# Kernel tuning notes

Hardware: AMD Instinct MI355X
Metric: run time of the kernel (lower is better)

Reference implementation:

```python
import jax, jax.numpy as jnp
import numpy as np

N, E, F_IN, HID, L, G, FFN = 100000, 1600000, 64, 128, 4, 512, 300
BN_EPS = 1e-5


def setup_inputs() -> dict:
    key = jax.random.key(0)
    ks = jax.random.split(key, 16)
    s = 0.05
    inp = {}
    inp["x"] = jax.random.normal(ks[0], (N, F_IN), dtype=jnp.float32)
    inp["edge_index"] = jax.random.randint(ks[1], (2, E), 0, N)
    inp["batch"] = jnp.sort(jax.random.randint(ks[2], (N,), 0, G))
    inp["enc_W"] = jax.random.normal(ks[3], (F_IN, HID), dtype=jnp.float32) * s
    inp["enc_b"] = jnp.zeros((HID,), jnp.float32)
    inp["Ws"] = jax.random.normal(ks[4], (L, HID, HID), dtype=jnp.float32) * s
    inp["bs"] = jnp.zeros((L, HID), jnp.float32)
    inp["bn_gamma"] = jnp.ones((L, HID), jnp.float32)
    inp["bn_beta"] = jnp.zeros((L, HID), jnp.float32)
    inp["bn_mean"] = jax.random.normal(ks[5], (L, HID), dtype=jnp.float32) * 0.01
    inp["bn_var"] = jnp.ones((L, HID), jnp.float32)
    inp["mlp_W0"] = jax.random.normal(ks[6], (HID, FFN), dtype=jnp.float32) * s
    inp["mlp_b0"] = jnp.zeros((FFN,), jnp.float32)
    inp["mlp_W1"] = jax.random.normal(ks[7], (FFN, FFN), dtype=jnp.float32) * s
    inp["mlp_b1"] = jnp.zeros((FFN,), jnp.float32)
    inp["mlp_W2"] = jax.random.normal(ks[8], (FFN, 1), dtype=jnp.float32) * s
    inp["mlp_b2"] = jnp.zeros((1,), jnp.float32)
    return inp


def reference(x, edge_index, batch, enc_W, enc_b, Ws, bs, bn_gamma, bn_beta,
              bn_mean, bn_var, mlp_W0, mlp_b0, mlp_W1, mlp_b1, mlp_W2, mlp_b2):
    # --- GCN normalization with self-loops (constant wrt params) ---
    loop = jnp.arange(N)
    row = jnp.concatenate([edge_index[0], loop])  # source
    col = jnp.concatenate([edge_index[1], loop])  # target (aggregation)
    deg = jax.ops.segment_sum(jnp.ones((E + N,), jnp.float32), col, num_segments=N)
    dinv = jnp.where(deg > 0, jax.lax.rsqrt(deg), 0.0)
    norm = dinv[row] * dinv[col]  # [E+N]

    # node encoder
    h = x @ enc_W + enc_b  # [N, HID]

    for i in range(L):
        h_prev = h
        # GCNConv: D^-1/2 (A+I) D^-1/2 (h W) + b
        hw = h @ Ws[i]
        msg = norm[:, None] * hw[row]                      # [E+N, HID]
        h = jax.ops.segment_sum(msg, col, num_segments=N) + bs[i]
        # BatchNorm1d (eval mode, running stats)
        h = (h - bn_mean[i]) * jax.lax.rsqrt(bn_var[i] + BN_EPS) * bn_gamma[i] + bn_beta[i]
        h = jax.nn.relu(h)
        if i > 0:
            h = h + h_prev

    # global mean pool over graphs
    sums = jax.ops.segment_sum(h, batch, num_segments=G)   # [G, HID]
    cnts = jax.ops.segment_sum(jnp.ones((N,), jnp.float32), batch, num_segments=G)
    gfeat = sums / jnp.maximum(cnts, 1.0)[:, None]

    # output MLP
    o = jax.nn.relu(gfeat @ mlp_W0 + mlp_b0)
    o = jax.nn.relu(o @ mlp_W1 + mlp_b1)
    return o @ mlp_W2 + mlp_b2  # [G, 1]
```

## Files before the change

kernel.cpp:

```cpp
#include <hip/hip_runtime.h>
#include <hip/hip_fp16.h>

#define NN 100000
#define NE 1600000
#define FIN 64
#define HID 128
#define NL 4
#define NG 512
#define FFN 300
#define BN_EPS 1e-5f
#define LDH 136
#define NB 512
#define NPB 196
#define CURPAD 16
#define CAP 4096

static inline size_t alignup(size_t x) { return (x + 255) & ~(size_t)255; }

struct half8 { __half2 h[4]; };

typedef _Float16 f16;
typedef __attribute__((ext_vector_type(4))) _Float16 f16x4;
typedef __attribute__((ext_vector_type(8))) _Float16 f16x8;
typedef __attribute__((ext_vector_type(4))) float f32x4;

__global__ void k_initcur(int* __restrict__ bcur) {
    int t = threadIdx.x;
    if (t < NB) bcur[t * CURPAD] = t * CAP;
}

__global__ __launch_bounds__(1024) void k_bscatter2(const int* __restrict__ row,
                                                    const int* __restrict__ col,
                                                    int* __restrict__ bcur,
                                                    int* __restrict__ ebuf) {
    __shared__ int hcnt[NB];
    __shared__ int hbase[NB];
    int t = threadIdx.x;
    int e0 = blockIdx.x * 4096;
    if (t < NB) hcnt[t] = 0;
    __syncthreads();
    #pragma unroll
    for (int k = 0; k < 4; ++k) {
        int e = e0 + k * 1024 + t;
        if (e < NE) atomicAdd(&hcnt[col[e] / NPB], 1);
    }
    __syncthreads();
    if (t < NB) {
        int c = hcnt[t];
        hbase[t] = (c > 0) ? atomicAdd(&bcur[t * CURPAD], c) : 0;
    }
    __syncthreads();
    if (t < NB) hcnt[t] = 0;
    __syncthreads();
    #pragma unroll
    for (int k = 0; k < 4; ++k) {
        int e = e0 + k * 1024 + t;
        if (e < NE) {
            int c = col[e];
            int b = c / NPB;
            int loc = atomicAdd(&hcnt[b], 1);
            ebuf[hbase[b] + loc] = row[e] | ((c - b * NPB) << 17);
        }
    }
}

__global__ __launch_bounds__(256) void k_binfill(const int* __restrict__ ebuf,
                                                 const int* __restrict__ bcur,
                                                 int* __restrict__ offs,
                                                 int* __restrict__ ends,
                                                 float* __restrict__ dinv,
                                                 int* __restrict__ csr_src) {
    __shared__ int cnt[NPB];
    __shared__ int scn[256];
    __shared__ int cur[NPB];
    int b = blockIdx.x, t = threadIdx.x;
    int lo = b * NPB;
    int hi = lo + NPB; if (hi > NN) hi = NN;
    int n = hi - lo;
    if (n <= 0) return;
    int s0 = b * CAP;
    int s1 = bcur[b * CURPAD];
    for (int i = t; i < NPB; i += 256) cnt[i] = 0;
    __syncthreads();
    for (int j = s0 + t; j < s1; j += 256)
        atomicAdd(&cnt[((unsigned)ebuf[j]) >> 17], 1);
    __syncthreads();
    int v = (t < n) ? cnt[t] : 0;
    scn[t] = v;
    __syncthreads();
    for (int off = 1; off < 256; off <<= 1) {
        int u = (t >= off) ? scn[t - off] : 0;
        __syncthreads();
        scn[t] += u;
        __syncthreads();
    }
    if (t < n) {
        int g = s0 + scn[t] - v;
        offs[lo + t] = g;
        ends[lo + t] = g + v;
        dinv[lo + t] = rsqrtf((float)(v + 1));
        cur[t] = g;
    }
    __syncthreads();
    for (int j = s0 + t; j < s1; j += 256) {
        int e = ebuf[j];
        int pos = atomicAdd(&cur[((unsigned)e) >> 17], 1);
        csr_src[pos] = e & 0x1FFFF;
    }
}

__global__ void k_convW(const float* __restrict__ Ws, const float* __restrict__ encW,
                        const float* __restrict__ bs, const float* __restrict__ gam,
                        const float* __restrict__ bet, const float* __restrict__ mean,
                        const float* __restrict__ var,
                        f16* __restrict__ wt, f16* __restrict__ wte,
                        float* __restrict__ pscale, float* __restrict__ pshift) {
    int tid = blockIdx.x * 256 + threadIdx.x;
    for (int i = tid; i < NL * HID * HID; i += 64 * 256) {
        int l = i >> 14, rem = i & 16383;
        int c = rem >> 7, k = rem & 127;
        wt[i] = (f16)Ws[(l << 14) + k * HID + c];
    }
    for (int i = tid; i < HID * FIN; i += 64 * 256) {
        int c = i >> 6, k = i & 63;
        wte[i] = (f16)encW[k * HID + c];
    }
    for (int i = tid; i < NL * HID; i += 64 * 256) {
        float rs = rsqrtf(var[i] + BN_EPS) * gam[i];
        pscale[i] = rs;
        pshift[i] = (bs[i] - mean[i]) * rs + bet[i];
    }
}

__global__ __launch_bounds__(256) void k_enc_mfma(const float* __restrict__ x,
                                                  const f16* __restrict__ wte,
                                                  const float* __restrict__ b,
                                                  __half* __restrict__ h) {
    __shared__ f16 sx[64 * 72];
    __shared__ f16 sw[128 * 72];
    int t = threadIdx.x;
    int row0 = blockIdx.x * 64;
    for (int idx = t; idx < 64 * 16; idx += 256) {
        int r = idx >> 4, c4 = (idx & 15) * 4;
        float4 v = {0.0f, 0.0f, 0.0f, 0.0f};
        if (row0 + r < NN) v = *(const float4*)(x + (size_t)(row0 + r) * FIN + c4);
        f16x4 o = {(f16)v.x, (f16)v.y, (f16)v.z, (f16)v.w};
        *(f16x4*)&sx[r * 72 + c4] = o;
    }
    for (int idx = t; idx < 128 * 8; idx += 256) {
        int c = idx >> 3, ch = (idx & 7) * 8;
        *(f16x8*)&sw[c * 72 + ch] = *(const f16x8*)(wte + c * FIN + ch);
    }
    __syncthreads();
    int w = t >> 6, lane = t & 63;
    int lrow = lane & 15, lk = (lane >> 4) * 8;
    f32x4 acc[8];
    #pragma unroll
    for (int ct = 0; ct < 8; ++ct) acc[ct] = (f32x4){0.0f, 0.0f, 0.0f, 0.0f};
    const f16* pa = &sx[(w * 16 + lrow) * 72 + lk];
    #pragma unroll
    for (int ks = 0; ks < 2; ++ks) {
        f16x8 a = *(const f16x8*)(pa + ks * 32);
        #pragma unroll
        for (int ct = 0; ct < 8; ++ct) {
            f16x8 bb = *(const f16x8*)&sw[(ct * 16 + lrow) * 72 + ks * 32 + lk];
            acc[ct] = __builtin_amdgcn_mfma_f32_16x16x32_f16(a, bb, acc[ct], 0, 0, 0);
        }
    }
    float bv[8];
    #pragma unroll
    for (int ct = 0; ct < 8; ++ct) bv[ct] = b[ct * 16 + lrow];
    int rbase = row0 + w * 16 + (lane >> 4) * 4;
    #pragma unroll
    for (int i = 0; i < 4; ++i) {
        int grow = rbase + i;
        if (grow < NN) {
            #pragma unroll
            for (int ct = 0; ct < 8; ++ct)
                h[(size_t)grow * HID + ct * 16 + lrow] = __float2half(acc[ct][i] + bv[ct]);
        }
    }
}

__global__ __launch_bounds__(256) void k_gemm_mfma(const __half* __restrict__ h,
                                                   const f16* __restrict__ wt,
                                                   const float* __restrict__ dinv,
                                                   __half* __restrict__ hw) {
    __shared__ f16 sh[64 * LDH];
    __shared__ f16 sw[128 * LDH];
    int t = threadIdx.x;
    int row0 = blockIdx.x * 64;
    for (int idx = t; idx < 64 * 16; idx += 256) {
        int r = idx >> 4, ch = (idx & 15) * 8;
        f16x8 v = {0, 0, 0, 0, 0, 0, 0, 0};
        if (row0 + r < NN) v = *(const f16x8*)(h + (size_t)(row0 + r) * HID + ch);
        *(f16x8*)&sh[r * LDH + ch] = v;
    }
    for (int idx = t; idx < 128 * 16; idx += 256) {
        int c = idx >> 4, ch = (idx & 15) * 8;
        *(f16x8*)&sw[c * LDH + ch] = *(const f16x8*)(wt + c * HID + ch);
    }
    __syncthreads();
    int w = t >> 6, lane = t & 63;
    int lrow = lane & 15, lk = (lane >> 4) * 8;
    f32x4 acc[8];
    #pragma unroll
    for (int ct = 0; ct < 8; ++ct) acc[ct] = (f32x4){0.0f, 0.0f, 0.0f, 0.0f};
    const f16* pa = &sh[(w * 16 + lrow) * LDH + lk];
    #pragma unroll
    for (int ks = 0; ks < 4; ++ks) {
        f16x8 a = *(const f16x8*)(pa + ks * 32);
        #pragma unroll
        for (int ct = 0; ct < 8; ++ct) {
            f16x8 b = *(const f16x8*)&sw[(ct * 16 + lrow) * LDH + ks * 32 + lk];
            acc[ct] = __builtin_amdgcn_mfma_f32_16x16x32_f16(a, b, acc[ct], 0, 0, 0);
        }
    }
    int rbase = row0 + w * 16 + (lane >> 4) * 4;
    #pragma unroll
    for (int i = 0; i < 4; ++i) {
        int grow = rbase + i;
        if (grow < NN) {
            float dv = dinv[grow];
            #pragma unroll
            for (int ct = 0; ct < 8; ++ct)
                hw[(size_t)grow * HID + ct * 16 + lrow] = __float2half(dv * acc[ct][i]);
        }
    }
}

__device__ __forceinline__ void add8(float* a, float4 raw) {
    const __half2* p = (const __half2*)&raw;
    #pragma unroll
    for (int q = 0; q < 4; ++q) {
        float2 u = __half22float2(p[q]);
        a[2 * q] += u.x;
        a[2 * q + 1] += u.y;
    }
}

__global__ __launch_bounds__(256) void k_gather(
    const int* __restrict__ offs, const int* __restrict__ ends,
    const int* __restrict__ csr_src,
    const float* __restrict__ dinv,
    const __half* __restrict__ hw, const __half* __restrict__ hprev,
    const float* __restrict__ pscale, const float* __restrict__ pshift,
    __half* __restrict__ hout, int with_res) {
    int node = (blockIdx.x * 256 + threadIdx.x) >> 6;
    if (node >= NN) return;
    int lane = threadIdx.x & 63;
    int grp = lane >> 4;
    int fb = (lane & 15) * 8;
    int s = offs[node], e = ends[node];
    float a[8] = {0, 0, 0, 0, 0, 0, 0, 0};
    int j = s + grp;
    for (; j + 12 < e; j += 16) {
        int s0 = csr_src[j], s1 = csr_src[j + 4], s2 = csr_src[j + 8], s3 = csr_src[j + 12];
        float4 r0 = *(const float4*)(hw + (size_t)s0 * HID + fb);
        float4 r1 = *(const float4*)(hw + (size_t)s1 * HID + fb);
        float4 r2 = *(const float4*)(hw + (size_t)s2 * HID + fb);
        float4 r3 = *(const float4*)(hw + (size_t)s3 * HID + fb);
        add8(a, r0); add8(a, r1); add8(a, r2); add8(a, r3);
    }
    for (; j + 4 < e; j += 8) {
        int s0 = csr_src[j], s1 = csr_src[j + 4];
        float4 r0 = *(const float4*)(hw + (size_t)s0 * HID + fb);
        float4 r1 = *(const float4*)(hw + (size_t)s1 * HID + fb);
        add8(a, r0); add8(a, r1);
    }
    for (; j < e; j += 4) {
        int s0 = csr_src[j];
        float4 r0 = *(const float4*)(hw + (size_t)s0 * HID + fb);
        add8(a, r0);
    }
    #pragma unroll
    for (int q = 0; q < 8; ++q) {
        a[q] += __shfl_xor(a[q], 16);
        a[q] += __shfl_xor(a[q], 32);
    }
    if (grp) return;
    float4 sraw = *(const float4*)(hw + (size_t)node * HID + fb);
    add8(a, sraw);
    float dc = dinv[node];
    float4 ps0 = *(const float4*)(pscale + fb), ps1 = *(const float4*)(pscale + fb + 4);
    float4 pf0 = *(const float4*)(pshift + fb), pf1 = *(const float4*)(pshift + fb + 4);
    float ps[8] = {ps0.x, ps0.y, ps0.z, ps0.w, ps1.x, ps1.y, ps1.z, ps1.w};
    float pf[8] = {pf0.x, pf0.y, pf0.z, pf0.w, pf1.x, pf1.y, pf1.z, pf1.w};
    float o[8];
    #pragma unroll
    for (int q = 0; q < 8; ++q)
        o[q] = fmaxf(dc * a[q] * ps[q] + pf[q], 0.0f);
    if (with_res) {
        float4 praw = *(const float4*)(hprev + (size_t)node * HID + fb);
        const __half2* pp = (const __half2*)&praw;
        #pragma unroll
        for (int q = 0; q < 4; ++q) {
            float2 p = __half22float2(pp[q]);
            o[2 * q] += p.x;
            o[2 * q + 1] += p.y;
        }
    }
    half8 ov;
    #pragma unroll
    for (int q = 0; q < 4; ++q)
        ov.h[q] = __floats2half2_rn(o[2 * q], o[2 * q + 1]);
    *(half8*)(hout + (size_t)node * HID + fb) = ov;
}

__device__ __forceinline__ int lower_bound_dev(const int* __restrict__ a, int n, int v) {
    int lo = 0, hi = n;
    while (lo < hi) {
        int m = (lo + hi) >> 1;
        if (a[m] < v) lo = m + 1; else hi = m;
    }
    return lo;
}

__global__ __launch_bounds__(256) void k_pool_seg(const __half* __restrict__ h,
                                                  const int* __restrict__ batch,
                                                  float* __restrict__ gfeat) {
    __shared__ int range[2];
    __shared__ float s[256];
    int g = blockIdx.x, t = threadIdx.x;
    if (t == 0) {
        range[0] = lower_bound_dev(batch, NN, g);
        range[1] = lower_bound_dev(batch, NN, g + 1);
    }
    __syncthreads();
    int start = range[0], end = range[1];
    int f = t & 127, half = t >> 7;
    float acc = 0.0f;
    for (int i = start + half; i < end; i += 2)
        acc += __half2float(h[(size_t)i * HID + f]);
    s[t] = acc;
    __syncthreads();
    if (t < 128) {
        float sum = s[t] + s[t + 128];
        float cnt = (float)(end - start);
        gfeat[(size_t)g * HID + t] = sum / fmaxf(cnt, 1.0f);
    }
}

__global__ void k_mlp0(const float* __restrict__ gfeat,
                       const float* __restrict__ W, const float* __restrict__ b,
                       float* __restrict__ out) {
    __shared__ float srow[HID];
    int g = blockIdx.x, t = threadIdx.x;
    if (t < HID) srow[t] = gfeat[(size_t)g * HID + t];
    __syncthreads();
    for (int j = t; j < FFN; j += 128) {
        float acc = b[j];
        for (int k = 0; k < HID; ++k) acc += srow[k] * W[k * FFN + j];
        out[(size_t)g * FFN + j] = fmaxf(acc, 0.0f);
    }
}

__global__ void k_mlp1(const float* __restrict__ in, const float* __restrict__ W,
                       const float* __restrict__ b, float* __restrict__ out) {
    __shared__ float srow[FFN];
    int g = blockIdx.x, t = threadIdx.x;
    for (int k = t; k < FFN; k += 128) srow[k] = in[(size_t)g * FFN + k];
    __syncthreads();
    for (int j = t; j < FFN; j += 128) {
        float acc = b[j];
        for (int k = 0; k < FFN; ++k) acc += srow[k] * W[k * FFN + j];
        out[(size_t)g * FFN + j] = fmaxf(acc, 0.0f);
    }
}

__global__ void k_mlp2(const float* __restrict__ in, const float* __restrict__ W,
                       const float* __restrict__ b, float* __restrict__ out) {
    int g = blockIdx.x, lane = threadIdx.x;
    float acc = 0.0f;
    for (int k = lane; k < FFN; k += 64) acc += in[(size_t)g * FFN + k] * W[k];
    for (int off = 32; off > 0; off >>= 1) acc += __shfl_down(acc, off);
    if (lane == 0) out[g] = acc + b[0];
}

extern "C" void kernel_launch(void* const* d_in, const int* in_sizes, int n_in,
                              void* d_out, int out_size, void* d_ws, size_t ws_size,
                              hipStream_t stream) {
    const float* x    = (const float*)d_in[0];
    const int*   ei   = (const int*)d_in[1];
    const int*   batch= (const int*)d_in[2];
    const float* encW = (const float*)d_in[3];
    const float* encb = (const float*)d_in[4];
    const float* Ws   = (const float*)d_in[5];
    const float* bs   = (const float*)d_in[6];
    const float* gam  = (const float*)d_in[7];
    const float* bet  = (const float*)d_in[8];
    const float* mean = (const float*)d_in[9];
    const float* var  = (const float*)d_in[10];
    const float* W0   = (const float*)d_in[11];
    const float* b0   = (const float*)d_in[12];
    const float* W1   = (const float*)d_in[13];
    const float* b1   = (const float*)d_in[14];
    const float* W2   = (const float*)d_in[15];
    const float* b2   = (const float*)d_in[16];
    float* out = (float*)d_out;

    char* w = (char*)d_ws;
    float*  dinv    = (float*)w;  w += alignup((size_t)NN * 4);
    int*    offs    = (int*)w;    w += alignup((size_t)NN * 4);
    int*    ends    = (int*)w;    w += alignup((size_t)NN * 4);
    int*    csr_src = (int*)w;    w += alignup((size_t)NB * CAP * 4);
    int*    bcur    = (int*)w;    w += alignup((size_t)NB * CURPAD * 4);
    int*    ebuf    = (int*)w;    w += alignup((size_t)NB * CAP * 4);
    __half* hA      = (__half*)w; w += alignup((size_t)NN * HID * 2);
    __half* hB      = (__half*)w; w += alignup((size_t)NN * HID * 2);
    __half* hw_     = (__half*)w; w += alignup((size_t)NN * HID * 2);
    f16*    wt      = (f16*)w;    w += alignup((size_t)NL * HID * HID * 2);
    f16*    wte     = (f16*)w;    w += alignup((size_t)HID * FIN * 2);
    float*  pscale  = (float*)w;  w += alignup((size_t)NL * HID * 4);
    float*  pshift  = (float*)w;  w += alignup((size_t)NL * HID * 4);
    float*  gfeat   = (float*)w;  w += alignup((size_t)NG * HID * 4);
    float*  m0      = (float*)w;  w += alignup((size_t)NG * FFN * 4);
    float*  m1      = (float*)w;  w += alignup((size_t)NG * FFN * 4);

    const int* row = ei;
    const int* col = ei + NE;

    k_initcur<<<1, NB, 0, stream>>>(bcur);
    k_bscatter2<<<(NE + 4095) / 4096, 1024, 0, stream>>>(row, col, bcur, ebuf);
    k_binfill<<<NB, 256, 0, stream>>>(ebuf, bcur, offs, ends, dinv, csr_src);

    k_convW<<<64, 256, 0, stream>>>(Ws, encW, bs, gam, bet, mean, var,
                                    wt, wte, pscale, pshift);
    k_enc_mfma<<<(NN + 63) / 64, 256, 0, stream>>>(x, wte, encb, hA);

    __half* hcur = hA;
    __half* hnext = hB;
    for (int l = 0; l < NL; ++l) {
        k_gemm_mfma<<<(NN + 63) / 64, 256, 0, stream>>>(hcur, wt + (size_t)l * HID * HID, dinv, hw_);
        k_gather<<<(NN * 64 + 255) / 256, 256, 0, stream>>>(
            offs, ends, csr_src, dinv, hw_, hcur,
            pscale + l * HID, pshift + l * HID,
            hnext, l > 0 ? 1 : 0);
        __half* tmp = hcur; hcur = hnext; hnext = tmp;
    }

    k_pool_seg<<<NG, 256, 0, stream>>>(hcur, batch, gfeat);
    k_mlp0<<<NG, 128, 0, stream>>>(gfeat, W0, b0, m0);
    k_mlp1<<<NG, 128, 0, stream>>>(m0, W1, b1, m1);
    k_mlp2<<<NG, 64, 0, stream>>>(m1, W2, b2, out);
}
```

Before: 492.7 us.

## Fuse encoder with first-layer GEMM and merge small launch kernels

The node encoder now feeds its fp16 output through shared memory directly into the layer-0 weight GEMM with dinv scaling, avoiding a full write and reread of the encoded feature matrix. The cursor-initialisation kernel is folded into the weight-conversion kernel, and the last two MLP layers are fused into one kernel with a block reduction. The fused encoder kernel uses much more shared memory, which may lower occupancy.

```diff
diff --git a/kernel.cpp b/kernel.cpp
--- a/kernel.cpp
+++ b/kernel.cpp
@@ -23,11 +23,6 @@
 typedef __attribute__((ext_vector_type(4))) _Float16 f16x4;
 typedef __attribute__((ext_vector_type(8))) _Float16 f16x8;
 typedef __attribute__((ext_vector_type(4))) float f32x4;
-
-__global__ void k_initcur(int* __restrict__ bcur) {
-    int t = threadIdx.x;
-    if (t < NB) bcur[t * CURPAD] = t * CAP;
-}
 
 __global__ __launch_bounds__(1024) void k_bscatter2(const int* __restrict__ row,
                                                     const int* __restrict__ col,
@@ -114,8 +109,10 @@
                         const float* __restrict__ bet, const float* __restrict__ mean,
                         const float* __restrict__ var,
                         f16* __restrict__ wt, f16* __restrict__ wte,
-                        float* __restrict__ pscale, float* __restrict__ pshift) {
+                        float* __restrict__ pscale, float* __restrict__ pshift,
+                        int* __restrict__ bcur) {
     int tid = blockIdx.x * 256 + threadIdx.x;
+    if (tid < NB) bcur[tid * CURPAD] = tid * CAP;
     for (int i = tid; i < NL * HID * HID; i += 64 * 256) {
         int l = i >> 14, rem = i & 16383;
         int c = rem >> 7, k = rem & 127;
@@ -132,12 +129,16 @@
     }
 }
 
-__global__ __launch_bounds__(256) void k_enc_mfma(const float* __restrict__ x,
-                                                  const f16* __restrict__ wte,
-                                                  const float* __restrict__ b,
-                                                  __half* __restrict__ h) {
+__global__ __launch_bounds__(256) void k_encgemm(const float* __restrict__ x,
+                                                 const f16* __restrict__ wte,
+                                                 const float* __restrict__ be,
+                                                 const f16* __restrict__ wt0,
+                                                 const float* __restrict__ dinv,
+                                                 __half* __restrict__ hw) {
     __shared__ f16 sx[64 * 72];
-    __shared__ f16 sw[128 * 72];
+    __shared__ f16 swe[128 * 72];
+    __shared__ f16 sh[64 * LDH];
+    __shared__ f16 sw0[128 * LDH];
     int t = threadIdx.x;
     int row0 = blockIdx.x * 64;
     for (int idx = t; idx < 64 * 16; idx += 256) {
@@ -149,7 +150,11 @@
     }
     for (int idx = t; idx < 128 * 8; idx += 256) {
         int c = idx >> 3, ch = (idx & 7) * 8;
-        *(f16x8*)&sw[c * 72 + ch] = *(const f16x8*)(wte + c * FIN + ch);
+        *(f16x8*)&swe[c * 72 + ch] = *(const f16x8*)(wte + c * FIN + ch);
+    }
+    for (int idx = t; idx < 128 * 16; idx += 256) {
+        int c = idx >> 4, ch = (idx & 15) * 8;
+        *(f16x8*)&sw0[c * LDH + ch] = *(const f16x8*)(wt0 + c * HID + ch);
     }
     __syncthreads();
     int w = t >> 6, lane = t & 63;
@@ -157,27 +162,51 @@
     f32x4 acc[8];
     #pragma unroll
     for (int ct = 0; ct < 8; ++ct) acc[ct] = (f32x4){0.0f, 0.0f, 0.0f, 0.0f};
-    const f16* pa = &sx[(w * 16 + lrow) * 72 + lk];
-    #pragma unroll
-    for (int ks = 0; ks < 2; ++ks) {
-        f16x8 a = *(const f16x8*)(pa + ks * 32);
+    {
+        const f16* pa = &sx[(w * 16 + lrow) * 72 + lk];
         #pragma unroll
-        for (int ct = 0; ct < 8; ++ct) {
-            f16x8 bb = *(const f16x8*)&sw[(ct * 16 + lrow) * 72 + ks * 32 + lk];
-            acc[ct] = __builtin_amdgcn_mfma_f32_16x16x32_f16(a, bb, acc[ct], 0, 0, 0);
+        for (int ks = 0; ks < 2; ++ks) {
+            f16x8 a = *(const f16x8*)(pa + ks * 32);
+            #pragma unroll
+            for (int ct = 0; ct < 8; ++ct) {
+                f16x8 bb = *(const f16x8*)&swe[(ct * 16 + lrow) * 72 + ks * 32 + lk];
+                acc[ct] = __builtin_amdgcn_mfma_f32_16x16x32_f16(a, bb, acc[ct], 0, 0, 0);
+            }
         }
     }
     float bv[8];
     #pragma unroll
-    for (int ct = 0; ct < 8; ++ct) bv[ct] = b[ct * 16 + lrow];
-    int rbase = row0 + w * 16 + (lane >> 4) * 4;
+    for (int ct = 0; ct < 8; ++ct) bv[ct] = be[ct * 16 + lrow];
+    int lr4 = w * 16 + (lane >> 4) * 4;
+    #pragma unroll
+    for (int i = 0; i < 4; ++i)
+        #pragma unroll
+        for (int ct = 0; ct < 8; ++ct)
+            sh[(lr4 + i) * LDH + ct * 16 + lrow] = (f16)(acc[ct][i] + bv[ct]);
+    __syncthreads();
+    #pragma unroll
+    for (int ct = 0; ct < 8; ++ct) acc[ct] = (f32x4){0.0f, 0.0f, 0.0f, 0.0f};
+    {
+        const f16* pa = &sh[(w * 16 + lrow) * LDH + lk];
+        #pragma unroll
+        for (int ks = 0; ks < 4; ++ks) {
+            f16x8 a = *(const f16x8*)(pa + ks * 32);
+            #pragma unroll
+            for (int ct = 0; ct < 8; ++ct) {
+                f16x8 b = *(const f16x8*)&sw0[(ct * 16 + lrow) * LDH + ks * 32 + lk];
+                acc[ct] = __builtin_amdgcn_mfma_f32_16x16x32_f16(a, b, acc[ct], 0, 0, 0);
+            }
+        }
+    }
+    int rbase = row0 + lr4;
     #pragma unroll
     for (int i = 0; i < 4; ++i) {
         int grow = rbase + i;
         if (grow < NN) {
+            float dv = dinv[grow];
             #pragma unroll
             for (int ct = 0; ct < 8; ++ct)
-                h[(size_t)grow * HID + ct * 16 + lrow] = __float2half(acc[ct][i] + bv[ct]);
+                hw[(size_t)grow * HID + ct * 16 + lrow] = __float2half(dv * acc[ct][i]);
         }
     }
 }
@@ -355,26 +384,30 @@
     }
 }
 
-__global__ void k_mlp1(const float* __restrict__ in, const float* __restrict__ W,
-                       const float* __restrict__ b, float* __restrict__ out) {
+__global__ void k_mlp12(const float* __restrict__ in, const float* __restrict__ W1,
+                        const float* __restrict__ b1, const float* __restrict__ W2,
+                        const float* __restrict__ b2, float* __restrict__ out) {
     __shared__ float srow[FFN];
+    __shared__ float s2[FFN];
+    __shared__ float red[128];
     int g = blockIdx.x, t = threadIdx.x;
     for (int k = t; k < FFN; k += 128) srow[k] = in[(size_t)g * FFN + k];
     __syncthreads();
     for (int j = t; j < FFN; j += 128) {
-        float acc = b[j];
-        for (int k = 0; k < FFN; ++k) acc += srow[k] * W[k * FFN + j];
-        out[(size_t)g * FFN + j] = fmaxf(acc, 0.0f);
-    }
-}
-
-__global__ void k_mlp2(const float* __restrict__ in, const float* __restrict__ W,
-                       const float* __restrict__ b, float* __restrict__ out) {
-    int g = blockIdx.x, lane = threadIdx.x;
-    float acc = 0.0f;
-    for (int k = lane; k < FFN; k += 64) acc += in[(size_t)g * FFN + k] * W[k];
-    for (int off = 32; off > 0; off >>= 1) acc += __shfl_down(acc, off);
-    if (lane == 0) out[g] = acc + b[0];
+        float acc = b1[j];
+        for (int k = 0; k < FFN; ++k) acc += srow[k] * W1[k * FFN + j];
+        s2[j] = fmaxf(acc, 0.0f);
+    }
+    __syncthreads();
+    float partial = 0.0f;
+    for (int k = t; k < FFN; k += 128) partial += s2[k] * W2[k];
+    red[t] = partial;
+    __syncthreads();
+    for (int off = 64; off > 0; off >>= 1) {
+        if (t < off) red[t] += red[t + off];
+        __syncthreads();
+    }
+    if (t == 0) out[g] = red[0] + b2[0];
 }
 
 extern "C" void kernel_launch(void* const* d_in, const int* in_sizes, int n_in,
@@ -415,32 +448,33 @@
     float*  pshift  = (float*)w;  w += alignup((size_t)NL * HID * 4);
     float*  gfeat   = (float*)w;  w += alignup((size_t)NG * HID * 4);
     float*  m0      = (float*)w;  w += alignup((size_t)NG * FFN * 4);
-    float*  m1      = (float*)w;  w += alignup((size_t)NG * FFN * 4);
 
     const int* row = ei;
     const int* col = ei + NE;
 
-    k_initcur<<<1, NB, 0, stream>>>(bcur);
+    k_convW<<<64, 256, 0, stream>>>(Ws, encW, bs, gam, bet, mean, var,
+                                    wt, wte, pscale, pshift, bcur);
+
     k_bscatter2<<<(NE + 4095) / 4096, 1024, 0, stream>>>(row, col, bcur, ebuf);
     k_binfill<<<NB, 256, 0, stream>>>(ebuf, bcur, offs, ends, dinv, csr_src);
 
-    k_convW<<<64, 256, 0, stream>>>(Ws, encW, bs, gam, bet, mean, var,
-                                    wt, wte, pscale, pshift);
-    k_enc_mfma<<<(NN + 63) / 64, 256, 0, stream>>>(x, wte, encb, hA);
+    k_encgemm<<<(NN + 63) / 64, 256, 0, stream>>>(x, wte, encb, wt, dinv, hw_);
 
     __half* hcur = hA;
     __half* hnext = hB;
-    for (int l = 0; l < NL; ++l) {
+    k_gather<<<(NN * 64 + 255) / 256, 256, 0, stream>>>(
+        offs, ends, csr_src, dinv, hw_, hcur ,
+        pscale, pshift, hcur, 0);
+    for (int l = 1; l < NL; ++l) {
         k_gemm_mfma<<<(NN + 63) / 64, 256, 0, stream>>>(hcur, wt + (size_t)l * HID * HID, dinv, hw_);
         k_gather<<<(NN * 64 + 255) / 256, 256, 0, stream>>>(
             offs, ends, csr_src, dinv, hw_, hcur,
             pscale + l * HID, pshift + l * HID,
-            hnext, l > 0 ? 1 : 0);
+            hnext, 1);
         __half* tmp = hcur; hcur = hnext; hnext = tmp;
     }
 
     k_pool_seg<<<NG, 256, 0, stream>>>(hcur, batch, gfeat);
     k_mlp0<<<NG, 128, 0, stream>>>(gfeat, W0, b0, m0);
-    k_mlp1<<<NG, 128, 0, stream>>>(m0, W1, b1, m1);
-    k_mlp2<<<NG, 64, 0, stream>>>(m1, W2, b2, out);
-}
+    k_mlp12<<<NG, 128, 0, stream>>>(m0, W1, b1, W2, b2, out);
+}
```

New measurement: 482.0 us. 1.02x faster.
